# Kernel optimization log

Hardware: AMD Instinct MI355X
Metric: run time of the kernel (lower is better)

Reference implementation:

```python
import jax, jax.numpy as jnp
import numpy as np

KERNELS = (2, 3, 6, 7)
ALPHA = 2.0
DT = 1.0  # time=1.0, step_size=1.0 -> one RK4 (3/8 rule) step, as torchdiffeq 'rk4'


def _conv(x, w, b):
    # x: [B,C,N,L], w: [O,I,1,k] -> valid conv over time axis
    y = jax.lax.conv_general_dilated(x, w, (1, 1), 'VALID',
                                     dimension_numbers=('NCHW', 'OIHW', 'NCHW'))
    return y + b[None, :, None, None]


def _inception(x, ws, bs):
    outs = [_conv(x, w, b) for w, b in zip(ws, bs)]
    L = outs[-1].shape[-1]  # shortest output (largest kernel=7)
    return jnp.concatenate([o[..., -L:] for o in outs], axis=1)


def _norm_adj(adj):
    A = adj + jnp.eye(adj.shape[0], dtype=adj.dtype)
    dinv = A.sum(1) ** -0.5
    return dinv[:, None] * A * dinv[None, :]  # D^-1/2 (A+I) D^-1/2


def _cgp(x, A_norm, mw, mb):
    f = lambda y: 0.5 * ALPHA * (jnp.einsum('ncwl,vw->ncvl', y, A_norm) - y)
    k1 = f(x)
    y2 = x + (DT / 3.0) * k1
    k2 = f(y2)
    y3 = x + DT * (k2 - k1 / 3.0)
    k3 = f(y3)
    y4 = x + DT * (k1 - k2 + k3)
    k4 = f(y4)
    yf = x + (DT / 8.0) * (k1 + 3.0 * (k2 + k3) + k4)
    # odefunc.out collects the state at each of the 4 f-evals, plus final state
    cat = jnp.concatenate([x, y2, y3, y4, yf], axis=1)  # [B, 5C, N, L]
    return _conv(cat, mw, mb)


def setup_inputs() -> dict:
    key = jax.random.key(0)
    B, C, N, T = 8, 64, 512, 64
    cq = C // 4
    ks = jax.random.split(key, 24)
    d = {
        'x': jax.random.normal(ks[0], (B, C, N, T), dtype=jnp.float32),
        'adj': jax.random.uniform(ks[1], (N, N), dtype=jnp.float32),
    }
    i = 2
    for branch in ('i1', 'i2'):
        for j, k in enumerate(KERNELS):
            d[f'{branch}w{j}'] = 0.1 * jax.random.normal(ks[i], (cq, C, 1, k), dtype=jnp.float32); i += 1
            d[f'{branch}b{j}'] = 0.1 * jax.random.normal(ks[i], (cq,), dtype=jnp.float32); i += 1
    d['m1w'] = 0.1 * jax.random.normal(ks[i], (C, 5 * C, 1, 1), dtype=jnp.float32); i += 1
    d['m1b'] = 0.1 * jax.random.normal(ks[i], (C,), dtype=jnp.float32); i += 1
    d['m2w'] = 0.1 * jax.random.normal(ks[i], (C, 5 * C, 1, 1), dtype=jnp.float32); i += 1
    d['m2b'] = 0.1 * jax.random.normal(ks[i], (C,), dtype=jnp.float32)
    return d


def reference(x, adj,
              i1w0, i1b0, i1w1, i1b1, i1w2, i1b2, i1w3, i1b3,
              i2w0, i2b0, i2w1, i2b1, i2w2, i2b2, i2w3, i2b3,
              m1w, m1b, m2w, m2b):
    T = x.shape[-1]  # receptive_field
    filt = jnp.tanh(_inception(x, (i1w0, i1w1, i1w2, i1w3), (i1b0, i1b1, i1b2, i1b3)))
    gate = jax.nn.sigmoid(_inception(x, (i2w0, i2w1, i2w2, i2w3), (i2b0, i2b1, i2b2, i2b3)))
    h = filt * gate  # dropout is identity in eval mode
    An = _norm_adj(adj)
    AnT = _norm_adj(adj.T)
    h = _cgp(h, An, m1w, m1b) + _cgp(h, AnT, m2w, m2b)
    pad = T - h.shape[-1]
    return jnp.pad(h, ((0, 0), (0, 0), (0, 0), (pad, 0)))
```

## Files before the change

kernel.cpp:

```cpp
#include <hip/hip_runtime.h>
#include <math.h>

#define NN 512
#define BB 8
#define CC 64
#define TT 64
#define LL 58
#define CL (CC*LL)
#define BCL (BB*CC*LL)
#define SZ ((size_t)NN*BCL)

typedef _Float16 half8 __attribute__((ext_vector_type(8)));
typedef _Float16 half4 __attribute__((ext_vector_type(4)));
typedef float f32x4 __attribute__((ext_vector_type(4)));

__global__ __launch_bounds__(64) void prep_adj(const float* __restrict__ adj,
                                               float* __restrict__ dinv1,
                                               float* __restrict__ dinv2){
  int v = blockIdx.x;
  int lane = threadIdx.x;
  float rs = 0.f, cs = 0.f;
  for (int w = lane; w < NN; w += 64){
    rs += adj[v*NN + w];
    cs += adj[w*NN + v];
  }
  for (int off = 32; off > 0; off >>= 1){
    rs += __shfl_down(rs, off);
    cs += __shfl_down(cs, off);
  }
  if (lane == 0){
    dinv1[v] = 1.f / sqrtf(rs + 1.f);
    dinv2[v] = 1.f / sqrtf(cs + 1.f);
  }
}

__global__ __launch_bounds__(256) void build_norm(const float* __restrict__ adj,
                                                  const float* __restrict__ dinv1,
                                                  const float* __restrict__ dinv2,
                                                  _Float16* __restrict__ An,
                                                  _Float16* __restrict__ AnT){
  int v = blockIdx.x;
  float d1v = dinv1[v], d2v = dinv2[v];
  for (int w = threadIdx.x; w < NN; w += 256){
    float diag = (v == w) ? 1.f : 0.f;
    An[v*NN + w]  = (_Float16)(d1v * (adj[v*NN + w] + diag) * dinv1[w] - diag);
    AnT[v*NN + w] = (_Float16)(d2v * (adj[w*NN + v] + diag) * dinv2[w] - diag);
  }
}

__global__ __launch_bounds__(256) void u_prep(const float* __restrict__ W1,
                                              const float* __restrict__ W2,
                                              _Float16* __restrict__ U1,
                                              _Float16* __restrict__ U2){
  const float coef[5][5] = {
    {1.f, 1.f, 1.f, 1.f, 1.f},
    {0.f, 1.f/3.f, 2.f/3.f, 1.f, 1.f},
    {0.f, 0.f, 1.f/3.f, 1.f/3.f, 0.5f},
    {0.f, 0.f, 0.f, 1.f/3.f, 1.f/6.f},
    {0.f, 0.f, 0.f, 0.f, 1.f/24.f}};
  int idx = blockIdx.x*256 + threadIdx.x;
  int o = idx / 320, rem = idx - o*320;
  int d = rem >> 6, c = rem & 63;
  float a1 = 0.f, a2 = 0.f;
  #pragma unroll
  for (int s = 0; s < 5; ++s){
    float cf = coef[d][s];
    a1 += cf * W1[o*320 + s*64 + c];
    a2 += cf * W2[o*320 + s*64 + c];
  }
  U1[idx] = (_Float16)a1;
  U2[idx] = (_Float16)a2;
}

__global__ __launch_bounds__(448) void wfg_prep(
    const float* __restrict__ w10, const float* __restrict__ w11,
    const float* __restrict__ w12, const float* __restrict__ w13,
    const float* __restrict__ w20, const float* __restrict__ w21,
    const float* __restrict__ w22, const float* __restrict__ w23,
    const float* __restrict__ b10, const float* __restrict__ b11,
    const float* __restrict__ b12, const float* __restrict__ b13,
    const float* __restrict__ b20, const float* __restrict__ b21,
    const float* __restrict__ b22, const float* __restrict__ b23,
    _Float16* __restrict__ WfG, float* __restrict__ biasFG){
  int r = blockIdx.x;
  int t = threadIdx.x;
  int qp = t >> 6, ic = t & 63;
  int gate = r >> 6;
  int j = (r >> 4) & 3;
  int oc = r & 15;
  const int kjs[4] = {2, 3, 6, 7};
  int kj = kjs[j];
  const float* wsel = gate ? ((j==0)?w20:(j==1)?w21:(j==2)?w22:w23)
                           : ((j==0)?w10:(j==1)?w11:(j==2)?w12:w13);
  int off = 7 - kj;
  float val = (qp >= off) ? wsel[(oc*64 + ic)*kj + (qp - off)] : 0.f;
  WfG[(size_t)r*448 + t] = (_Float16)val;
  if (t == 0){
    const float* bsel = gate ? ((j==0)?b20:(j==1)?b21:(j==2)?b22:b23)
                             : ((j==0)?b10:(j==1)?b11:(j==2)?b12:b13);
    biasFG[r] = bsel[oc];
  }
}

__global__ __launch_bounds__(256) void xt_prep(const float* __restrict__ x,
                                               _Float16* __restrict__ xTg){
  __shared__ float T[64][65];
  int n = blockIdx.x;
  int b = blockIdx.y;
  int tid = threadIdx.x;
  #pragma unroll
  for (int r = 0; r < 4; ++r){
    int f = tid + r*256;
    int ic = f >> 4, t4 = f & 15;
    float4 v = *(const float4*)&x[(((size_t)(b*64 + ic))*512 + n)*64 + t4*4];
    T[ic][t4*4+0] = v.x; T[ic][t4*4+1] = v.y;
    T[ic][t4*4+2] = v.z; T[ic][t4*4+3] = v.w;
  }
  __syncthreads();
  #pragma unroll
  for (int r = 0; r < 2; ++r){
    int f = tid + r*256;
    int t = f >> 3, ch = f & 7;
    half8 hv;
    #pragma unroll
    for (int q2 = 0; q2 < 8; ++q2) hv[q2] = (_Float16)T[ch*8 + q2][t];
    *(half8*)&xTg[(((size_t)(b*64 + t))*512 + n)*64 + ch*8] = hv;
  }
}

__global__ __launch_bounds__(256, 3) void inception_mfma(
    const _Float16* __restrict__ xTg,
    const _Float16* __restrict__ WfG,
    const float* __restrict__ biasFG,
    _Float16* __restrict__ S_h){
  __shared__ _Float16 X[13*32*64];
  int nt = blockIdx.x;
  int lt = blockIdx.y;
  int b  = blockIdx.z;
  int n0 = nt*32, l0 = lt*7;
  int tid = threadIdx.x;

  int sch = tid & 7, sn = (tid >> 3) & 31;
  #pragma unroll
  for (int r = 0; r < 13; ++r){
    int t = l0 + r;
    half8 v = {};
    if (t < 64)
      v = *(const half8*)&xTg[(((size_t)(b*64 + t))*512 + n0 + sn)*64 + sch*8];
    *(half8*)&X[(size_t)(r*256 + sn*8 + (sch ^ (sn & 7)))*8] = v;
  }

  int w = tid >> 6, lane = tid & 63;
  int m = lane & 15, kg = lane >> 4;

  half8 wF[14], wG[14];
  const _Float16* wb = WfG + (size_t)(w*16 + m)*448 + kg*8;
  #pragma unroll
  for (int s = 0; s < 14; ++s){
    wF[s] = *(const half8*)(wb + s*32);
    wG[s] = *(const half8*)(wb + (size_t)64*448 + s*32);
  }
  f32x4 bF = *(const f32x4*)&biasFG[w*16 + kg*4];
  f32x4 bG = *(const f32x4*)&biasFG[64 + w*16 + kg*4];

  __syncthreads();

  for (int ll = 0; ll < 7; ++ll){
    f32x4 aF0 = {}, aF1 = {}, aG0 = {}, aG1 = {};
    #pragma unroll
    for (int s = 0; s < 14; ++s){
      int t = ll + (s >> 1);
      int c0 = (s & 1)*4 + kg;
      half8 b0 = *(half8*)&X[(size_t)(t*256 + m*8        + (c0 ^ (m & 7)))*8];
      half8 b1 = *(half8*)&X[(size_t)(t*256 + (16+m)*8   + (c0 ^ (m & 7)))*8];
      aF0 = __builtin_amdgcn_mfma_f32_16x16x32_f16(wF[s], b0, aF0, 0, 0, 0);
      aG0 = __builtin_amdgcn_mfma_f32_16x16x32_f16(wG[s], b0, aG0, 0, 0, 0);
      aF1 = __builtin_amdgcn_mfma_f32_16x16x32_f16(wF[s], b1, aF1, 0, 0, 0);
      aG1 = __builtin_amdgcn_mfma_f32_16x16x32_f16(wG[s], b1, aG1, 0, 0, 0);
    }
    int l = l0 + ll;
    if (l < LL){
      #pragma unroll
      for (int rr = 0; rr < 4; ++rr){
        int c = w*16 + kg*4 + rr;
        float F0 = aF0[rr] + bF[rr];
        float G0 = aG0[rr] + bG[rr];
        float F1 = aF1[rr] + bF[rr];
        float G1 = aG1[rr] + bG[rr];
        float h0 = (2.f*__builtin_amdgcn_rcpf(1.f + __expf(-2.f*F0)) - 1.f)
                 * __builtin_amdgcn_rcpf(1.f + __expf(-G0));
        float h1 = (2.f*__builtin_amdgcn_rcpf(1.f + __expf(-2.f*F1)) - 1.f)
                 * __builtin_amdgcn_rcpf(1.f + __expf(-G1));
        size_t base = ((size_t)(b*64 + c)*LL + l)*NN + n0;
        S_h[base + m]      = (_Float16)h0;
        S_h[base + 16 + m] = (_Float16)h1;
      }
    }
  }
}

__device__ __forceinline__ void gll16(const _Float16* g, _Float16* l){
  __builtin_amdgcn_global_load_lds(
      (const __attribute__((address_space(1))) unsigned int*)g,
      (__attribute__((address_space(3))) unsigned int*)l, 16, 0, 0);
}
#define BAR() asm volatile("s_barrier" ::: "memory")

__global__ __launch_bounds__(512, 2) void gemm_z2(
    int nx,
    const _Float16* __restrict__ A0, const _Float16* __restrict__ B0,
    _Float16* __restrict__ O0,
    const _Float16* __restrict__ A1, const _Float16* __restrict__ B1,
    _Float16* __restrict__ O1){
  __shared__ _Float16 L[65536];

  int bid = blockIdx.x;
  int q8 = gridDim.x >> 3;
  int virt = (bid & 7)*q8 + (bid >> 3);
  int y = virt & 1;
  int pair = virt >> 1;
  int x = pair % nx;
  int z = pair / nx;

  const _Float16* __restrict__ A = z ? A1 : A0;
  const _Float16* __restrict__ B = z ? B1 : B0;
  _Float16* __restrict__ O = z ? O1 : O0;

  const int m0 = x * 256;
  const int v0 = y * 256;
  const int tid = threadIdx.x;
  const int ww = tid >> 6;
  const int lane = tid & 63;
  const int lr = lane & 15;
  const int kg = lane >> 4;
  const int wv = ww >> 2;
  const int wm = ww & 3;

  const int srow = lane >> 2;
  const int gch  = (lane & 3) ^ (srow & 3);
  const _Float16* gAb = A + (size_t)(v0 + ww*32 + srow)*NN + gch*8;
  const _Float16* gBb = B + (size_t)(m0 + ww*32 + srow)*NN + gch*8;

  #define STAGE_A(tt, kk)                                                   \
    { char* l_ = (char*)L + (size_t)((tt)&1)*65536 + (size_t)(kk)*16384     \
                 + ww*2048;                                                 \
      const _Float16* g_ = gAb + (tt)*64 + (kk)*32;                         \
      gll16(g_,         (_Float16*)l_);                                     \
      gll16(g_ + 16*NN, (_Float16*)(l_ + 1024)); }
  #define STAGE_B(tt, kk)                                                   \
    { char* l_ = (char*)L + (size_t)((tt)&1)*65536 + 32768                  \
                 + (size_t)(kk)*16384 + ww*2048;                            \
      const _Float16* g_ = gBb + (tt)*64 + (kk)*32;                         \
      gll16(g_,         (_Float16*)l_);                                     \
      gll16(g_ + 16*NN, (_Float16*)(l_ + 1024)); }

  const int csw = (kg ^ (lr & 3)) * 16;
  const int aR = (wv*128 + lr)*64 + csw;
  const int bR = 32768 + (wm*64 + lr)*64 + csw;

  half8 af[4], bf[4];
  f32x4 acc[8][4] = {};

  #define LOADS_A(buf, kk, ih)                                              \
    _Pragma("unroll")                                                       \
    for (int q_ = 0; q_ < 4; ++q_)                                          \
      af[q_] = *(const half8*)((char*)L + (buf)*65536 + (kk)*16384          \
                               + aR + ((ih)*4 + q_)*1024);
  #define LOADS_B(buf, kk)                                                  \
    _Pragma("unroll")                                                       \
    for (int q_ = 0; q_ < 4; ++q_)                                          \
      bf[q_] = *(const half8*)((char*)L + (buf)*65536 + (kk)*16384          \
                               + bR + q_*1024);
  #define MFMA16(ih)                                                        \
    __builtin_amdgcn_s_setprio(1);                                          \
    _Pragma("unroll")                                                       \
    for (int i_ = 0; i_ < 4; ++i_)                                          \
      _Pragma("unroll")                                                     \
      for (int j_ = 0; j_ < 4; ++j_)                                        \
        acc[(ih)*4 + i_][j_] = __builtin_amdgcn_mfma_f32_16x16x32_f16(      \
            af[i_], bf[j_], acc[(ih)*4 + i_][j_], 0, 0, 0);                 \
    __builtin_amdgcn_s_setprio(0);

  STAGE_A(0,0) STAGE_B(0,0)
  STAGE_A(0,1) STAGE_B(0,1)
  STAGE_A(1,0) STAGE_B(1,0)
  asm volatile("s_waitcnt vmcnt(8)" ::: "memory");
  BAR();

  #pragma unroll
  for (int kt = 0; kt < 8; ++kt){
    const int buf = kt & 1;
    LOADS_A(buf, 0, 0); LOADS_B(buf, 0);
    if (kt + 1 < 8) STAGE_A(kt+1, 1)
    BAR();
    MFMA16(0);
    BAR();
    LOADS_A(buf, 0, 1);
    if (kt + 1 < 8) STAGE_B(kt+1, 1)
    BAR();
    MFMA16(1);
    if (kt < 7) { asm volatile("s_waitcnt vmcnt(8)" ::: "memory"); }
    else        { asm volatile("s_waitcnt vmcnt(0)" ::: "memory"); }
    BAR();
    LOADS_A(buf, 1, 0); LOADS_B(buf, 1);
    if (kt + 2 < 8) STAGE_A(kt+2, 0)
    BAR();
    MFMA16(0);
    BAR();
    LOADS_A(buf, 1, 1);
    if (kt + 2 < 8) STAGE_B(kt+2, 0)
    BAR();
    MFMA16(1);
    if (kt < 6)      { asm volatile("s_waitcnt vmcnt(8)" ::: "memory"); }
    else if (kt == 6){ asm volatile("s_waitcnt vmcnt(4)" ::: "memory"); }
    BAR();
  }
  #undef STAGE_A
  #undef STAGE_B
  #undef LOADS_A
  #undef LOADS_B
  #undef MFMA16

  char* Lw = (char*)L + ww*16384;
  #pragma unroll
  for (int j = 0; j < 4; ++j){
    int row = j*16 + lr;
    #pragma unroll
    for (int i = 0; i < 8; ++i){
      int c = (i*4 + kg) ^ ((lr & 7)*4);
      half4 oq;
      #pragma unroll
      for (int rr = 0; rr < 4; ++rr) oq[rr] = (_Float16)acc[i][j][rr];
      *(half4*)(Lw + row*256 + c*8) = oq;
    }
  }
  #pragma unroll
  for (int s = 0; s < 16; ++s){
    int row = s*4 + kg;
    int cc = (2*lr) ^ ((row & 7)*4);
    half8 hv = *(const half8*)(Lw + row*256 + cc*8);
    *(half8*)&O[(size_t)(m0 + wm*64 + row)*NN + v0 + wv*128 + lr*8] = hv;
  }
}

template<int PASS>
__global__ __launch_bounds__(256, 3) void combine_mfma(
    const _Float16* __restrict__ Sh, const _Float16* __restrict__ S2,
    const _Float16* __restrict__ S3, const _Float16* __restrict__ S4,
    const _Float16* __restrict__ Sf,
    const _Float16* __restrict__ Wc,
    const float* __restrict__ bias,
    _Float16* __restrict__ tmp){
  __shared__ __align__(16) _Float16 Xt[256*64];
  __shared__ float Bsh[64];
  int v0 = blockIdx.x * 256;
  int l  = blockIdx.y;
  int b  = blockIdx.z;
  int tid = threadIdx.x;
  int w = tid >> 6, lane = tid & 63;
  int lr = lane & 15, kg = lane >> 4;

  if (tid < 64) Bsh[tid] = bias[tid];

  const int c0  = ((tid >> 3) & 7) * 8;
  const int lv0 = (tid & 7) * 8 + w * 64;
  const int wslot = (c0 >> 3) ^ (((lv0 >> 3) & 1) << 2);
  const int rx = ((lr >> 3) & 1) << 2;

  const _Float16* Sarr[5] = {Sh, S2, S3, S4, Sf};
  f32x4 acc[4][4] = {};

  for (int kt = 0; kt < 5; ++kt){
    const _Float16* S = Sarr[kt];
    unsigned xr[8][4];
    const _Float16* gbase = &S[((size_t)(b*64 + c0)*58 + l)*512 + v0 + lv0];
    #pragma unroll
    for (int r = 0; r < 8; ++r)
      *(uint4*)xr[r] = *(const uint4*)(gbase + (size_t)r*58*512);

    __syncthreads();

    #pragma unroll
    for (int q = 0; q < 8; ++q){
      const unsigned sel = (q & 1) ? 0x07060302u : 0x05040100u;
      const int d2 = q >> 1;
      uint4 y;
      y.x = __builtin_amdgcn_perm(xr[1][d2], xr[0][d2], sel);
      y.y = __builtin_amdgcn_perm(xr[3][d2], xr[2][d2], sel);
      y.z = __builtin_amdgcn_perm(xr[5][d2], xr[4][d2], sel);
      y.w = __builtin_amdgcn_perm(xr[7][d2], xr[6][d2], sel);
      *(uint4*)((char*)Xt + (lv0 + q)*128 + wslot*16) = y;
    }

    half8 aW[2][4];
    #pragma unroll
    for (int ks = 0; ks < 2; ++ks)
      #pragma unroll
      for (int jj = 0; jj < 4; ++jj)
        aW[ks][jj] = *(const half8*)&Wc[(size_t)(jj*16 + lr)*320
                                        + kt*64 + ks*32 + kg*8];

    __syncthreads();

    #pragma unroll
    for (int ks = 0; ks < 2; ++ks){
      #pragma unroll
      for (int vt = 0; vt < 4; ++vt){
        half8 bf = *(const half8*)((char*)Xt + (w*64 + vt*16 + lr)*128
                                   + ((ks*4 + kg) ^ rx)*16);
        #pragma unroll
        for (int jj = 0; jj < 4; ++jj)
          acc[vt][jj] = __builtin_amdgcn_mfma_f32_16x16x32_f16(
              aW[ks][jj], bf, acc[vt][jj], 0, 0, 0);
      }
    }
  }

  size_t rowbase = ((size_t)b*58 + l)*64;
  #pragma unroll
  for (int jj = 0; jj < 4; ++jj){
    #pragma unroll
    for (int rr = 0; rr < 4; ++rr){
      int o = jj*16 + kg*4 + rr;
      float bv = Bsh[o];
      size_t obase = (rowbase + o)*512 + v0 + w*64 + lr;
      #pragma unroll
      for (int vt = 0; vt < 4; ++vt){
        float val = acc[vt][jj][rr] + bv;
        size_t addr = obase + vt*16;
        if (PASS == 0) tmp[addr] = (_Float16)val;
        else           tmp[addr] = (_Float16)((float)tmp[addr] + val);
      }
    }
  }
}

__global__ __launch_bounds__(256) void untranspose(const _Float16* __restrict__ tmp,
                                                   float* __restrict__ out){
  __shared__ float T[58][65];
  int o = blockIdx.x;
  int b = blockIdx.y;
  int v0 = blockIdx.z * 64;
  int t = threadIdx.x;
  for (int idx = t; idx < 58*64; idx += 256){
    int lr = idx >> 6, vv = idx & 63;
    T[lr][vv] = (float)tmp[((size_t)(b*58 + lr)*64 + o)*NN + v0 + vv];
  }
  __syncthreads();
  #pragma unroll
  for (int i = 0; i < 16; ++i){
    int c = t + i*256;
    int vv = c >> 6, tt = c & 63;
    float val = (tt < 6) ? 0.f : T[tt - 6][vv];
    out[((size_t)(b*64 + o)*NN + v0 + vv)*TT + tt] = val;
  }
}

extern "C" void kernel_launch(void* const* d_in, const int* in_sizes, int n_in,
                              void* d_out, int out_size, void* d_ws, size_t ws_size,
                              hipStream_t stream){
  const float* x   = (const float*)d_in[0];
  const float* adj = (const float*)d_in[1];
  const float* w1[4] = {(const float*)d_in[2],  (const float*)d_in[4],
                        (const float*)d_in[6],  (const float*)d_in[8]};
  const float* b1[4] = {(const float*)d_in[3],  (const float*)d_in[5],
                        (const float*)d_in[7],  (const float*)d_in[9]};
  const float* w2[4] = {(const float*)d_in[10], (const float*)d_in[12],
                        (const float*)d_in[14], (const float*)d_in[16]};
  const float* b2[4] = {(const float*)d_in[11], (const float*)d_in[13],
                        (const float*)d_in[15], (const float*)d_in[17]};
  const float* m1w = (const float*)d_in[18];
  const float* m1b = (const float*)d_in[19];
  const float* m2w = (const float*)d_in[20];
  const float* m2b = (const float*)d_in[21];

  char* wsb = (char*)d_ws;
  float* dinv1 = (float*)(wsb);
  float* dinv2 = (float*)(wsb + 2048);
  _Float16* U1  = (_Float16*)(wsb + 4096);
  _Float16* U2  = (_Float16*)(wsb + 4096 + 40960);
  _Float16* Mn  = (_Float16*)(wsb + 167936);
  _Float16* MnT = (_Float16*)(wsb + 167936 + 524288);
  size_t sbytes = SZ * 2;
  char* sbase = wsb + 1216512;
  _Float16* S_h = (_Float16*)(sbase);
  _Float16* S2  = (_Float16*)(sbase + sbytes);
  _Float16* S3  = (_Float16*)(sbase + 2*sbytes);
  _Float16* S4  = (_Float16*)(sbase + 3*sbytes);
  _Float16* S5  = (_Float16*)(sbase + 4*sbytes);
  _Float16* tmp = (_Float16*)(sbase + 5*sbytes);
  _Float16* xTg = S2;
  _Float16* WfG = (_Float16*)(sbase + 6*sbytes);
  float* biasFG = (float*)(sbase + 6*sbytes + 114688);
  _Float16* M2  = (_Float16*)(sbase + 6*sbytes + 131072);
  _Float16* MT2 = (_Float16*)(sbase + 6*sbytes + 131072 + 524288);
  float* out = (float*)d_out;

  prep_adj<<<NN, 64, 0, stream>>>(adj, dinv1, dinv2);
  build_norm<<<NN, 256, 0, stream>>>(adj, dinv1, dinv2, Mn, MnT);
  gemm_z2<<<8, 512, 0, stream>>>(2, MnT, Mn, M2, Mn, MnT, MT2);
  u_prep<<<80, 256, 0, stream>>>(m1w, m2w, U1, U2);
  wfg_prep<<<128, 448, 0, stream>>>(
      w1[0],w1[1],w1[2],w1[3], w2[0],w2[1],w2[2],w2[3],
      b1[0],b1[1],b1[2],b1[3], b2[0],b2[1],b2[2],b2[3], WfG, biasFG);
  xt_prep<<<dim3(NN, BB), 256, 0, stream>>>(x, xTg);
  inception_mfma<<<dim3(16, 9, 8), 256, 0, stream>>>(xTg, WfG, biasFG, S_h);

  dim3 gc(2, LL, BB);
  for (int pass = 0; pass < 2; ++pass){
    const _Float16* Mp  = pass ? MnT : Mn;
    const _Float16* Mp2 = pass ? MT2 : M2;
    gemm_z2<<<464, 512, 0, stream>>>(116, Mp, S_h, S2, Mp2, S_h, S3);
    gemm_z2<<<464, 512, 0, stream>>>(116, Mp2, S2, S4, Mp2, S3, S5);
    if (pass == 0)
      combine_mfma<0><<<gc, 256, 0, stream>>>(S_h, S2, S3, S4, S5, U1, m1b, tmp);
    else
      combine_mfma<1><<<gc, 256, 0, stream>>>(S_h, S2, S3, S4, S5, U2, m2b, tmp);
  }
  untranspose<<<dim3(64, 8, 8), 256, 0, stream>>>(tmp, out);
}
```

Measured before the change: 471.6 us.

## Shrink gemm_z2 tile to 256x128 with 4 waves and simpler K-pipeline

Reworks the graph-propagation GEMM from 512-thread blocks with 256x256 output tiles to 256-thread blocks with 256x128 tiles. Each wave now covers 128x64 and loads 8 A fragments per K step of 32. The two-level interleaved staging schedule becomes a plain double-buffered K loop of 16 steps, and the LDS swizzle is changed. Grid sizes double, which is meant to improve occupancy and load balance on the GPU, at the cost of more re-reading of the A operand and less reuse per block.

```diff
diff --git a/kernel.cpp b/kernel.cpp
--- a/kernel.cpp
+++ b/kernel.cpp
@@ -206,13 +206,13 @@
 }
 #define BAR() asm volatile("s_barrier" ::: "memory")
 
-__global__ __launch_bounds__(512, 2) void gemm_z2(
+__global__ __launch_bounds__(256, 2) void gemm_z2(
     int nx,
     const _Float16* __restrict__ A0, const _Float16* __restrict__ B0,
     _Float16* __restrict__ O0,
     const _Float16* __restrict__ A1, const _Float16* __restrict__ B1,
     _Float16* __restrict__ O1){
-  __shared__ _Float16 L[65536];
+  __shared__ _Float16 L[32768];
 
   int bid = blockIdx.x;
   int q8 = gridDim.x >> 3;
@@ -226,100 +226,74 @@
   const _Float16* __restrict__ B = z ? B1 : B0;
   _Float16* __restrict__ O = z ? O1 : O0;
 
-  const int m0 = x * 256;
+  const int m0 = x * 128;
   const int v0 = y * 256;
   const int tid = threadIdx.x;
   const int ww = tid >> 6;
   const int lane = tid & 63;
   const int lr = lane & 15;
   const int kg = lane >> 4;
-  const int wv = ww >> 2;
-  const int wm = ww & 3;
+  const int wvq = ww & 1;
+  const int wmq = ww >> 1;
 
   const int srow = lane >> 2;
-  const int gch  = (lane & 3) ^ (srow & 3);
-  const _Float16* gAb = A + (size_t)(v0 + ww*32 + srow)*NN + gch*8;
+  const int gch  = ((lane & 3) - ((lane >> 3) & 3)) & 3;
+  const _Float16* gAb = A + (size_t)(v0 + ww*64 + srow)*NN + gch*8;
   const _Float16* gBb = B + (size_t)(m0 + ww*32 + srow)*NN + gch*8;
 
-  #define STAGE_A(tt, kk)                                                   \
-    { char* l_ = (char*)L + (size_t)((tt)&1)*65536 + (size_t)(kk)*16384     \
-                 + ww*2048;                                                 \
-      const _Float16* g_ = gAb + (tt)*64 + (kk)*32;                         \
-      gll16(g_,         (_Float16*)l_);                                     \
-      gll16(g_ + 16*NN, (_Float16*)(l_ + 1024)); }
-  #define STAGE_B(tt, kk)                                                   \
-    { char* l_ = (char*)L + (size_t)((tt)&1)*65536 + 32768                  \
-                 + (size_t)(kk)*16384 + ww*2048;                            \
-      const _Float16* g_ = gBb + (tt)*64 + (kk)*32;                         \
-      gll16(g_,         (_Float16*)l_);                                     \
-      gll16(g_ + 16*NN, (_Float16*)(l_ + 1024)); }
-
-  const int csw = (kg ^ (lr & 3)) * 16;
-  const int aR = (wv*128 + lr)*64 + csw;
-  const int bR = 32768 + (wm*64 + lr)*64 + csw;
-
-  half8 af[4], bf[4];
+  #define STAGE(buf, kt)                                                    \
+    { char* lA_ = (char*)L + (buf)*24576 + ww*4096;                         \
+      char* lB_ = (char*)L + (buf)*24576 + 16384 + ww*2048;                 \
+      const _Float16* gA_ = gAb + (kt)*32;                                  \
+      const _Float16* gB_ = gBb + (kt)*32;                                  \
+      _Pragma("unroll")                                                     \
+      for (int s_ = 0; s_ < 4; ++s_)                                        \
+        gll16(gA_ + (size_t)s_*16*NN, (_Float16*)(lA_ + s_*1024));          \
+      _Pragma("unroll")                                                     \
+      for (int s_ = 0; s_ < 2; ++s_)                                        \
+        gll16(gB_ + (size_t)s_*16*NN, (_Float16*)(lB_ + s_*1024)); }
+
+  const int slot = (kg + (lr >> 1)) & 3;
+  const int aOff = (wvq*128 + lr)*64 + slot*16;
+  const int bOff = 16384 + (wmq*64 + lr)*64 + slot*16;
+
+  half8 af[8], bf[4];
   f32x4 acc[8][4] = {};
 
-  #define LOADS_A(buf, kk, ih)                                              \
-    _Pragma("unroll")                                                       \
-    for (int q_ = 0; q_ < 4; ++q_)                                          \
-      af[q_] = *(const half8*)((char*)L + (buf)*65536 + (kk)*16384          \
-                               + aR + ((ih)*4 + q_)*1024);
-  #define LOADS_B(buf, kk)                                                  \
-    _Pragma("unroll")                                                       \
-    for (int q_ = 0; q_ < 4; ++q_)                                          \
-      bf[q_] = *(const half8*)((char*)L + (buf)*65536 + (kk)*16384          \
-                               + bR + q_*1024);
-  #define MFMA16(ih)                                                        \
-    __builtin_amdgcn_s_setprio(1);                                          \
-    _Pragma("unroll")                                                       \
-    for (int i_ = 0; i_ < 4; ++i_)                                          \
-      _Pragma("unroll")                                                     \
-      for (int j_ = 0; j_ < 4; ++j_)                                        \
-        acc[(ih)*4 + i_][j_] = __builtin_amdgcn_mfma_f32_16x16x32_f16(      \
-            af[i_], bf[j_], acc[(ih)*4 + i_][j_], 0, 0, 0);                 \
+  STAGE(0, 0)
+  STAGE(1, 1)
+  asm volatile("s_waitcnt vmcnt(6)" ::: "memory");
+  BAR();
+
+  #pragma unroll
+  for (int kt = 0; kt < 16; ++kt){
+    const int buf = kt & 1;
+    char* lb = (char*)L + buf*24576;
+    #pragma unroll
+    for (int i = 0; i < 8; ++i) af[i] = *(const half8*)(lb + aOff + i*1024);
+    #pragma unroll
+    for (int j = 0; j < 4; ++j) bf[j] = *(const half8*)(lb + bOff + j*1024);
+    asm volatile("s_waitcnt lgkmcnt(0)" ::: "memory");
+    BAR();
+    if (kt + 2 < 16) STAGE(buf, kt + 2)
+
+    __builtin_amdgcn_s_setprio(1);
+    #pragma unroll
+    for (int i = 0; i < 8; ++i)
+      #pragma unroll
+      for (int j = 0; j < 4; ++j)
+        acc[i][j] = __builtin_amdgcn_mfma_f32_16x16x32_f16(af[i], bf[j], acc[i][j], 0, 0, 0);
     __builtin_amdgcn_s_setprio(0);
 
-  STAGE_A(0,0) STAGE_B(0,0)
-  STAGE_A(0,1) STAGE_B(0,1)
-  STAGE_A(1,0) STAGE_B(1,0)
-  asm volatile("s_waitcnt vmcnt(8)" ::: "memory");
-  BAR();
-
-  #pragma unroll
-  for (int kt = 0; kt < 8; ++kt){
-    const int buf = kt & 1;
-    LOADS_A(buf, 0, 0); LOADS_B(buf, 0);
-    if (kt + 1 < 8) STAGE_A(kt+1, 1)
-    BAR();
-    MFMA16(0);
-    BAR();
-    LOADS_A(buf, 0, 1);
-    if (kt + 1 < 8) STAGE_B(kt+1, 1)
-    BAR();
-    MFMA16(1);
-    if (kt < 7) { asm volatile("s_waitcnt vmcnt(8)" ::: "memory"); }
-    else        { asm volatile("s_waitcnt vmcnt(0)" ::: "memory"); }
-    BAR();
-    LOADS_A(buf, 1, 0); LOADS_B(buf, 1);
-    if (kt + 2 < 8) STAGE_A(kt+2, 0)
-    BAR();
-    MFMA16(0);
-    BAR();
-    LOADS_A(buf, 1, 1);
-    if (kt + 2 < 8) STAGE_B(kt+2, 0)
-    BAR();
-    MFMA16(1);
-    if (kt < 6)      { asm volatile("s_waitcnt vmcnt(8)" ::: "memory"); }
-    else if (kt == 6){ asm volatile("s_waitcnt vmcnt(4)" ::: "memory"); }
-    BAR();
-  }
-  #undef STAGE_A
-  #undef STAGE_B
-  #undef LOADS_A
-  #undef LOADS_B
-  #undef MFMA16
+    if (kt < 14){
+      asm volatile("s_waitcnt vmcnt(6)" ::: "memory");
+      BAR();
+    } else if (kt == 14){
+      asm volatile("s_waitcnt vmcnt(0)" ::: "memory");
+      BAR();
+    }
+  }
+  #undef STAGE
 
   char* Lw = (char*)L + ww*16384;
   #pragma unroll
@@ -339,7 +313,7 @@
     int row = s*4 + kg;
     int cc = (2*lr) ^ ((row & 7)*4);
     half8 hv = *(const half8*)(Lw + row*256 + cc*8);
-    *(half8*)&O[(size_t)(m0 + wm*64 + row)*NN + v0 + wv*128 + lr*8] = hv;
+    *(half8*)&O[(size_t)(m0 + wmq*64 + row)*NN + v0 + wvq*128 + lr*8] = hv;
   }
 }
 
@@ -498,7 +472,7 @@
 
   prep_adj<<<NN, 64, 0, stream>>>(adj, dinv1, dinv2);
   build_norm<<<NN, 256, 0, stream>>>(adj, dinv1, dinv2, Mn, MnT);
-  gemm_z2<<<8, 512, 0, stream>>>(2, MnT, Mn, M2, Mn, MnT, MT2);
+  gemm_z2<<<16, 256, 0, stream>>>(4, MnT, Mn, M2, Mn, MnT, MT2);
   u_prep<<<80, 256, 0, stream>>>(m1w, m2w, U1, U2);
   wfg_prep<<<128, 448, 0, stream>>>(
       w1[0],w1[1],w1[2],w1[3], w2[0],w2[1],w2[2],w2[3],
@@ -510,8 +484,8 @@
   for (int pass = 0; pass < 2; ++pass){
     const _Float16* Mp  = pass ? MnT : Mn;
     const _Float16* Mp2 = pass ? MT2 : M2;
-    gemm_z2<<<464, 512, 0, stream>>>(116, Mp, S_h, S2, Mp2, S_h, S3);
-    gemm_z2<<<464, 512, 0, stream>>>(116, Mp2, S2, S4, Mp2, S3, S5);
+    gemm_z2<<<928, 256, 0, stream>>>(232, Mp, S_h, S2, Mp2, S_h, S3);
+    gemm_z2<<<928, 256, 0, stream>>>(232, Mp2, S2, S4, Mp2, S3, S5);
     if (pass == 0)
       combine_mfma<0><<<gc, 256, 0, stream>>>(S_h, S2, S3, S4, S5, U1, m1b, tmp);
     else
```

Result: faster. 460.7 us (-2.3%).
